# Kernel tuning notes

Hardware: AMD Instinct MI355X
Metric: run time of the kernel (lower is better)

The kernel has to match this reference:

```python
import jax, jax.numpy as jnp
import numpy as np

EPS = 1e-6

def _ln(x, w, b):
    m = x.mean(-1, keepdims=True)
    v = ((x - m) ** 2).mean(-1, keepdims=True)
    return (x - m) / jnp.sqrt(v + EPS) * w + b

def setup_inputs() -> dict:
    key = jax.random.key(0)
    ks = jax.random.split(key, 16)
    N, P, C, M = 8192, 64, 128, 4096
    MW = M * P  # 262144 gathered tokens
    A, BL = 131072, 65536
    x = jax.random.normal(ks[0], (N, P, C), dtype=jnp.float32)
    index_window = jax.random.permutation(ks[1], N)[:M]
    index_partition = jax.random.permutation(ks[2], MW)
    perm2 = jax.random.permutation(ks[3], MW)
    asy_index = perm2[:A]
    blocked_index = perm2[A:A + BL]
    p = lambda k, sh: 0.02 * jax.random.normal(k, sh, dtype=jnp.float32)
    return {
        "x": x,
        "index_window": index_window,
        "index_partition": index_partition,
        "asy_index": asy_index,
        "blocked_index": blocked_index,
        "M": M,
        "B": N,
        "ln1_w": jnp.ones((C,), jnp.float32), "ln1_b": jnp.zeros((C,), jnp.float32),
        "qkv_w": p(ks[4], (C, 3 * C)), "qkv_b": jnp.zeros((3 * C,), jnp.float32),
        "proj_w": p(ks[5], (C, C)), "proj_b": jnp.zeros((C,), jnp.float32),
        "gamma1": jnp.full((C,), 1e-1, jnp.float32),
        "ln2_w": jnp.ones((C,), jnp.float32), "ln2_b": jnp.zeros((C,), jnp.float32),
        "mlp_w1": p(ks[6], (C, 4 * C)), "mlp_b1": jnp.zeros((4 * C,), jnp.float32),
        "mlp_w2": p(ks[7], (4 * C, C)), "mlp_b2": jnp.zeros((C,), jnp.float32),
        "gamma2": jnp.full((C,), 1e-1, jnp.float32),
    }

def reference(x, index_window, index_partition, asy_index, blocked_index, M, B,
              ln1_w, ln1_b, qkv_w, qkv_b, proj_w, proj_b, gamma1,
              ln2_w, ln2_b, mlp_w1, mlp_b1, mlp_w2, mlp_b2, gamma2):
    N, P, C = x.shape
    H, dh = 4, 32
    scale = dh ** -0.5
    MW = index_partition.shape[0]
    x = _ln(x, ln1_w, ln1_b)                      # first_norm over whole input
    X = x                                          # (N, P, C)
    xw = x[index_window].reshape(-1, C)            # gather windows -> (MW, C)
    XX = xw
    xa = _ln(xw[asy_index], ln1_w, ln1_b)          # second norm on asy tokens
    xw = xw.at[asy_index].set(xa)
    shortcut = xa                                  # (A, C)
    xp = xw[index_partition].reshape(M, -1, C)     # (M, P, C) attention groups
    qkv = (xp @ qkv_w + qkv_b).reshape(M, P, H, 3 * dh).transpose(0, 2, 1, 3)
    q, k, v = jnp.split(qkv, 3, axis=3)            # each (M, H, P, dh)
    attn = jnp.einsum('mhqd,mhkd->mhqk', q, k) * scale
    # scatter scores keyed by key-token into flat map, mask blocked keys, gather back
    am = jnp.zeros((MW, P, H), attn.dtype)
    am = am.at[index_partition].set(jnp.transpose(attn, (0, 3, 2, 1)).reshape(MW, P, H))
    am = am.at[blocked_index].set(-10000.0)
    attn = jnp.transpose(am[index_partition].reshape(M, P, P, H), (0, 3, 2, 1))
    attn = jax.nn.softmax(attn, axis=-1)
    o = jnp.einsum('mhqk,mhkd->mhqd', attn, v).transpose(0, 2, 1, 3).reshape(M, P, C)
    o = o @ proj_w + proj_b
    XX = XX.at[index_partition].set(o.reshape(-1, C))
    y = XX[asy_index]
    # sub_layers: [ls1, droppath(id), ln2, mlp, ls2, droppath(id)]
    y = y * gamma1                                 # i=0
    y = shortcut + y                               # i=1 residual
    shortcut = y
    y2 = _ln(y, ln2_w, ln2_b)                      # i=2
    y2 = jax.nn.gelu(y2 @ mlp_w1 + mlp_b1, approximate=False) @ mlp_w2 + mlp_b2  # i=3
    y2 = y2 * gamma2                               # i=4
    y = shortcut + y2                              # i=5 residual
    XX = XX.at[asy_index].set(y)
    XX = XX.at[blocked_index].set(X[index_window].reshape(-1, C)[blocked_index])
    X = X.at[index_window].set(XX.reshape(M, -1, C))
    return X
```

## Files before the change

kernel.cpp:

```cpp
#include <hip/hip_runtime.h>
#include <hip/hip_bf16.h>
#include <math.h>

#define N_   8192
#define P_   64
#define C_   128
#define M_   4096
#define MW_  (M_ * P_)
#define A_   131072
#define BL_  65536
#define NROWS_ (N_ * P_)

typedef __attribute__((ext_vector_type(8))) __bf16 bf16x8;
typedef __attribute__((ext_vector_type(4))) float f32x4;
typedef __attribute__((ext_vector_type(2))) __bf16 bf16x2;

__device__ __forceinline__ float wave_sum(float v) {
#pragma unroll
  for (int o = 32; o > 0; o >>= 1) v += __shfl_xor(v, o, 64);
  return v;
}

__global__ __launch_bounds__(256) void k_set8(unsigned char* p, int n) {
  int i = blockIdx.x * 256 + threadIdx.x;
  if (i < n) p[i] = 0;
}
__global__ __launch_bounds__(256) void k_scatter2(unsigned char* p,
                                                  const int* __restrict__ ia,
                                                  const int* __restrict__ ib) {
  int i = blockIdx.x * 256 + threadIdx.x;
  if (i < A_) p[ia[i]] = 1;
  else {
    int j = i - A_;
    if (j < BL_) p[ib[j]] = 2;
  }
}

__global__ __launch_bounds__(256) void k_prep(const float* __restrict__ qkvw,
                                              const float* __restrict__ projw,
                                              const float* __restrict__ w1,
                                              const float* __restrict__ w2,
                                              __bf16* __restrict__ qkvt,
                                              __bf16* __restrict__ projt,
                                              __bf16* __restrict__ w1t,
                                              __bf16* __restrict__ w2t) {
  int i = blockIdx.x * 256 + threadIdx.x;
  if (i < 384 * 128) {
    int col = i >> 7, row = i & 127;
    qkvt[i] = (__bf16)qkvw[row * 384 + col];
  } else if (i < 384 * 128 + 128 * 128) {
    int j = i - 384 * 128;
    int col = j >> 7, row = j & 127;
    projt[j] = (__bf16)projw[row * 128 + col];
  } else if (i < 384 * 128 + 128 * 128 + 512 * 128) {
    int j = i - 384 * 128 - 128 * 128;
    int col = j >> 7, row = j & 127;
    w1t[j] = (__bf16)w1[row * 512 + col];
  } else {
    int j = i - 384 * 128 - 128 * 128 - 512 * 128;
    int col = j >> 9, row = j & 511;
    w2t[j] = (__bf16)w2[row * 128 + col];
  }
}

__global__ __launch_bounds__(256) void k_ln_all(const float* __restrict__ x,
                                                const float* __restrict__ w,
                                                const float* __restrict__ b,
                                                float* __restrict__ out) {
  int hw = threadIdx.x >> 5, l = threadIdx.x & 31;
  size_t row = (size_t)blockIdx.x * 8 + hw;
  float4 v = ((const float4*)(x + row * 128))[l];
  float s = (v.x + v.y) + (v.z + v.w);
#pragma unroll
  for (int o = 1; o < 32; o <<= 1) s += __shfl_xor(s, o, 64);
  float mean = s * (1.0f / 128.0f);
  float d0 = v.x - mean, d1 = v.y - mean, d2 = v.z - mean, d3 = v.w - mean;
  float q = (d0 * d0 + d1 * d1) + (d2 * d2 + d3 * d3);
#pragma unroll
  for (int o = 1; o < 32; o <<= 1) q += __shfl_xor(q, o, 64);
  float inv = rsqrtf(q * (1.0f / 128.0f) + 1e-6f);
  float4 wv = ((const float4*)w)[l];
  float4 bv = ((const float4*)b)[l];
  float4 o4;
  o4.x = d0 * inv * wv.x + bv.x;
  o4.y = d1 * inv * wv.y + bv.y;
  o4.z = d2 * inv * wv.z + bv.z;
  o4.w = d3 * inv * wv.w + bv.w;
  ((float4*)(out + row * 128))[l] = o4;
}

__global__ __launch_bounds__(512, 6) void k_attn(
    const int* __restrict__ iw,
    const int* __restrict__ ip, const unsigned char* __restrict__ flags,
    const float* __restrict__ ln1w, const float* __restrict__ ln1b,
    const __bf16* __restrict__ qkvt, const float* __restrict__ qkvb,
    const __bf16* __restrict__ projt, const float* __restrict__ projb,
    float* out) {
  __shared__ __align__(16) __bf16 XV[64 * 132];
  __shared__ __align__(16) __bf16 scratch[4 * 4352];
  __shared__ int srow[64];
  __shared__ unsigned char fl[64];

  const int tid = threadIdx.x;
  const int w = tid >> 6, lane = tid & 63;
  const int quad = lane >> 4, cl = lane & 15;
  const int h = w >> 1, mh = w & 1;
  const int m = blockIdx.x;

  if (tid < 64) {
    int s = ip[(m << 6) + tid];
    fl[tid] = flags[s];
    srow[tid] = iw[s >> 6] * 64 + (s & 63);
  }
  __syncthreads();

  __bf16* Xs = XV;
  const float lw0 = ln1w[2 * lane], lw1 = ln1w[2 * lane + 1];
  const float lb0 = ln1b[2 * lane], lb1 = ln1b[2 * lane + 1];

  {
    float2 xv[8];
#pragma unroll
    for (int ii = 0; ii < 8; ++ii) {
      int r = w * 8 + ii;
      xv[ii] = ((const float2*)(out + (size_t)srow[r] * 128))[lane];
    }
#pragma unroll
    for (int ii = 0; ii < 8; ++ii) {
      int r = w * 8 + ii;
      float y0 = xv[ii].x, y1 = xv[ii].y;
      if (fl[r] == 1) {
        float mean = wave_sum(y0 + y1) * (1.0f / 128.0f);
        float d0 = y0 - mean, d1 = y1 - mean;
        float inv = rsqrtf(wave_sum(d0 * d0 + d1 * d1) * (1.0f / 128.0f) + 1e-6f);
        y0 = d0 * inv * lw0 + lb0;
        y1 = d1 * inv * lw1 + lb1;
      }
      bf16x2 p2;
      p2[0] = (__bf16)y0; p2[1] = (__bf16)y1;
      *(bf16x2*)&Xs[r * 132 + 2 * lane] = p2;
    }
  }
  __syncthreads();

  __bf16* wsc = scratch + h * 4352;
  __bf16* Qs  = wsc;
  __bf16* Ks  = wsc + 2176;
  __bf16* Vts = XV + h * 2112;
  __bf16* Ps  = wsc;
  __bf16* Os  = wsc;

  bf16x8 af[2][4];
#pragma unroll
  for (int mtl = 0; mtl < 2; ++mtl)
#pragma unroll
    for (int kt = 0; kt < 4; ++kt)
      af[mtl][kt] = *(const bf16x8*)&Xs[((mh * 2 + mtl) * 16 + cl) * 132 + kt * 32 + quad * 8];
  __syncthreads();

#pragma unroll
  for (int t = 0; t < 3; ++t) {
#pragma unroll
    for (int nt = 0; nt < 2; ++nt) {
      int col = h * 96 + t * 32 + nt * 16 + cl;
      bf16x8 bfr[4];
#pragma unroll
      for (int kt = 0; kt < 4; ++kt)
        bfr[kt] = *(const bf16x8*)&qkvt[(size_t)col * 128 + kt * 32 + quad * 8];
      float bias = qkvb[col];
      __builtin_amdgcn_s_setprio(1);
#pragma unroll
      for (int mtl = 0; mtl < 2; ++mtl) {
        int mt = mh * 2 + mtl;
        f32x4 acc = {bias, bias, bias, bias};
#pragma unroll
        for (int kt = 0; kt < 4; ++kt)
          acc = __builtin_amdgcn_mfma_f32_16x16x32_bf16(af[mtl][kt], bfr[kt], acc, 0, 0, 0);
        if (t == 0) {
#pragma unroll
          for (int r = 0; r < 4; ++r)
            Qs[(mt * 16 + quad * 4 + r) * 34 + nt * 16 + cl] = (__bf16)acc[r];
        } else if (t == 1) {
#pragma unroll
          for (int r = 0; r < 4; ++r)
            Ks[(mt * 16 + quad * 4 + r) * 34 + nt * 16 + cl] = (__bf16)acc[r];
        } else {
#pragma unroll
          for (int r = 0; r < 4; ++r)
            Vts[(nt * 16 + cl) * 66 + mt * 16 + quad * 4 + r] = (__bf16)acc[r];
        }
      }
      __builtin_amdgcn_s_setprio(0);
    }
  }
  __syncthreads();

  f32x4 sc4[2][4];
  {
    bf16x8 bk[4];
#pragma unroll
    for (int nt = 0; nt < 4; ++nt)
      bk[nt] = *(const bf16x8*)&Ks[(nt * 16 + cl) * 34 + quad * 8];
    bf16x8 aq[2];
#pragma unroll
    for (int mtl = 0; mtl < 2; ++mtl)
      aq[mtl] = *(const bf16x8*)&Qs[((mh * 2 + mtl) * 16 + cl) * 34 + quad * 8];
    __builtin_amdgcn_s_setprio(1);
#pragma unroll
    for (int mtl = 0; mtl < 2; ++mtl)
#pragma unroll
      for (int nt = 0; nt < 4; ++nt) {
        f32x4 z = {0.f, 0.f, 0.f, 0.f};
        sc4[mtl][nt] = __builtin_amdgcn_mfma_f32_16x16x32_bf16(aq[mtl], bk[nt], z, 0, 0, 0);
      }
    __builtin_amdgcn_s_setprio(0);
  }
  __syncthreads();

  const float scale = 0.17677669529663687f;
  bool blk[4];
#pragma unroll
  for (int nt = 0; nt < 4; ++nt) blk[nt] = (fl[nt * 16 + cl] == 2);
#pragma unroll
  for (int mtl = 0; mtl < 2; ++mtl)
#pragma unroll
    for (int nt = 0; nt < 4; ++nt)
#pragma unroll
      for (int r = 0; r < 4; ++r) {
        float v = sc4[mtl][nt][r];
        sc4[mtl][nt][r] = blk[nt] ? -10000.0f : v * scale;
      }
#pragma unroll
  for (int mtl = 0; mtl < 2; ++mtl) {
#pragma unroll
    for (int r = 0; r < 4; ++r) {
      float mx = fmaxf(fmaxf(sc4[mtl][0][r], sc4[mtl][1][r]),
                       fmaxf(sc4[mtl][2][r], sc4[mtl][3][r]));
#pragma unroll
      for (int off = 1; off < 16; off <<= 1) mx = fmaxf(mx, __shfl_xor(mx, off, 64));
      float e0 = __expf(sc4[mtl][0][r] - mx);
      float e1 = __expf(sc4[mtl][1][r] - mx);
      float e2 = __expf(sc4[mtl][2][r] - mx);
      float e3 = __expf(sc4[mtl][3][r] - mx);
      float sm = (e0 + e1) + (e2 + e3);
#pragma unroll
      for (int off = 1; off < 16; off <<= 1) sm += __shfl_xor(sm, off, 64);
      float inv = 1.0f / sm;
      int row = (mh * 2 + mtl) * 16 + quad * 4 + r;
      Ps[row * 68 +  0 + cl] = (__bf16)(e0 * inv);
      Ps[row * 68 + 16 + cl] = (__bf16)(e1 * inv);
      Ps[row * 68 + 32 + cl] = (__bf16)(e2 * inv);
      Ps[row * 68 + 48 + cl] = (__bf16)(e3 * inv);
    }
  }

  f32x4 oacc[2][2];
  {
    bf16x8 bv[2][2];
#pragma unroll
    for (int nt = 0; nt < 2; ++nt)
#pragma unroll
      for (int kt = 0; kt < 2; ++kt)
        bv[nt][kt] = *(const bf16x8*)&Vts[(nt * 16 + cl) * 66 + kt * 32 + quad * 8];
    __builtin_amdgcn_s_setprio(1);
#pragma unroll
    for (int mtl = 0; mtl < 2; ++mtl) {
      int mt = mh * 2 + mtl;
      bf16x8 ap0 = *(const bf16x8*)&Ps[(mt * 16 + cl) * 68 + quad * 8];
      bf16x8 ap1 = *(const bf16x8*)&Ps[(mt * 16 + cl) * 68 + 32 + quad * 8];
#pragma unroll
      for (int nt = 0; nt < 2; ++nt) {
        f32x4 z = {0.f, 0.f, 0.f, 0.f};
        z = __builtin_amdgcn_mfma_f32_16x16x32_bf16(ap0, bv[nt][0], z, 0, 0, 0);
        z = __builtin_amdgcn_mfma_f32_16x16x32_bf16(ap1, bv[nt][1], z, 0, 0, 0);
        oacc[mtl][nt] = z;
      }
    }
    __builtin_amdgcn_s_setprio(0);
  }
  __syncthreads();
#pragma unroll
  for (int mtl = 0; mtl < 2; ++mtl)
#pragma unroll
    for (int nt = 0; nt < 2; ++nt)
#pragma unroll
      for (int r = 0; r < 4; ++r)
        Os[((mh * 2 + mtl) * 16 + quad * 4 + r) * 36 + nt * 16 + cl] = (__bf16)oacc[mtl][nt][r];
  __syncthreads();

  {
    const int col = w * 16 + cl;
    bf16x8 bpr[4];
#pragma unroll
    for (int kt = 0; kt < 4; ++kt)
      bpr[kt] = *(const bf16x8*)&projt[(size_t)col * 128 + kt * 32 + quad * 8];
    const float pb = projb[col];
#pragma unroll
    for (int mt = 0; mt < 4; ++mt) {
      f32x4 acc = {pb, pb, pb, pb};
#pragma unroll
      for (int kt = 0; kt < 4; ++kt) {
        const __bf16* op = scratch + kt * 4352;
        bf16x8 a = *(const bf16x8*)&op[(mt * 16 + cl) * 36 + quad * 8];
        acc = __builtin_amdgcn_mfma_f32_16x16x32_bf16(a, bpr[kt], acc, 0, 0, 0);
      }
#pragma unroll
      for (int r = 0; r < 4; ++r) {
        int row = mt * 16 + quad * 4 + r;
        if (fl[row] != 2)
          out[(size_t)srow[row] * 128 + col] = acc[r];
      }
    }
  }
}

__global__ __launch_bounds__(256, 4) void k_mlp(
    const float* __restrict__ x, const int* __restrict__ iw,
    const int* __restrict__ ia,
    const float* __restrict__ ln1w, const float* __restrict__ ln1b,
    const float* __restrict__ g1,
    const float* __restrict__ ln2w, const float* __restrict__ ln2b,
    const __bf16* __restrict__ w1t, const float* __restrict__ b1,
    const __bf16* __restrict__ w2t, const float* __restrict__ b2,
    const float* __restrict__ g2,
    float* out) {
  __shared__ __align__(16) __bf16 y2s[64 * 136];
  __shared__ __align__(16) __bf16 hb[64 * 136];
  __shared__ int wrs[64];

  const int tid = threadIdx.x;
  const int w = tid >> 6, lane = tid & 63;
  const int quad = lane >> 4, cl = lane & 15;

  if (tid < 64) {
    int s = ia[(blockIdx.x << 6) + tid];
    wrs[tid] = iw[s >> 6] * 64 + (s & 63);
  }
  __syncthreads();

  const float lw0 = ln1w[2 * lane], lw1 = ln1w[2 * lane + 1];
  const float lb0 = ln1b[2 * lane], lb1 = ln1b[2 * lane + 1];
  const float g1a = g1[2 * lane], g1b = g1[2 * lane + 1];
  const float l2w0 = ln2w[2 * lane], l2w1 = ln2w[2 * lane + 1];
  const float l2b0 = ln2b[2 * lane], l2b1 = ln2b[2 * lane + 1];

  for (int half = 0; half < 2; ++half) {
    float2 xv[8], ov[8];
#pragma unroll
    for (int ii = 0; ii < 8; ++ii) {
      int r = w + 4 * (half * 8 + ii);
      size_t wr = (size_t)wrs[r];
      xv[ii] = ((const float2*)(x + wr * 128))[lane];
      ov[ii] = ((const float2*)(out + wr * 128))[lane];
    }
#pragma unroll
    for (int ii = 0; ii < 8; ++ii) {
      int r = w + 4 * (half * 8 + ii);
      float mean = wave_sum(xv[ii].x + xv[ii].y) * (1.0f / 128.0f);
      float d0 = xv[ii].x - mean, d1 = xv[ii].y - mean;
      float inv = rsqrtf(wave_sum(d0 * d0 + d1 * d1) * (1.0f / 128.0f) + 1e-6f);
      float y0 = d0 * inv * lw0 + lb0, y1 = d1 * inv * lw1 + lb1;
      mean = wave_sum(y0 + y1) * (1.0f / 128.0f);
      d0 = y0 - mean; d1 = y1 - mean;
      inv = rsqrtf(wave_sum(d0 * d0 + d1 * d1) * (1.0f / 128.0f) + 1e-6f);
      float xa0 = d0 * inv * lw0 + lb0, xa1 = d1 * inv * lw1 + lb1;
      float yv0 = xa0 + g1a * ov[ii].x;
      float yv1 = xa1 + g1b * ov[ii].y;
      ((float2*)(out + (size_t)wrs[r] * 128))[lane] = make_float2(yv0, yv1);
      mean = wave_sum(yv0 + yv1) * (1.0f / 128.0f);
      d0 = yv0 - mean; d1 = yv1 - mean;
      inv = rsqrtf(wave_sum(d0 * d0 + d1 * d1) * (1.0f / 128.0f) + 1e-6f);
      bf16x2 p2;
      p2[0] = (__bf16)(d0 * inv * l2w0 + l2b0);
      p2[1] = (__bf16)(d1 * inv * l2w1 + l2b1);
      *(bf16x2*)&y2s[r * 136 + 2 * lane] = p2;
    }
  }
  __threadfence_block();
  __syncthreads();

  f32x4 zacc[4][2];
#pragma unroll
  for (int nt = 0; nt < 2; ++nt) {
    float bb = b2[w * 32 + nt * 16 + cl];
#pragma unroll
    for (int mt = 0; mt < 4; ++mt) zacc[mt][nt] = (f32x4){bb, bb, bb, bb};
  }

  for (int ch = 0; ch < 4; ++ch) {
#pragma unroll
    for (int nt = 0; nt < 2; ++nt) {
      int col = ch * 128 + w * 32 + nt * 16 + cl;
      bf16x8 bfr[4];
#pragma unroll
      for (int kt = 0; kt < 4; ++kt)
        bfr[kt] = *(const bf16x8*)&w1t[(size_t)col * 128 + kt * 32 + quad * 8];
      float bias = b1[col];
      __builtin_amdgcn_s_setprio(1);
#pragma unroll
      for (int mt = 0; mt < 4; ++mt) {
        f32x4 acc = {bias, bias, bias, bias};
#pragma unroll
        for (int kt = 0; kt < 4; ++kt) {
          bf16x8 a = *(const bf16x8*)&y2s[(mt * 16 + cl) * 136 + kt * 32 + quad * 8];
          acc = __builtin_amdgcn_mfma_f32_16x16x32_bf16(a, bfr[kt], acc, 0, 0, 0);
        }
#pragma unroll
        for (int r = 0; r < 4; ++r) {
          float a = acc[r];
          float g = a * 0.5f * (1.0f + erff(a * 0.70710678118654752f));
          hb[(mt * 16 + quad * 4 + r) * 136 + w * 32 + nt * 16 + cl] = (__bf16)g;
        }
      }
      __builtin_amdgcn_s_setprio(0);
    }
    __syncthreads();
#pragma unroll
    for (int nt = 0; nt < 2; ++nt) {
      int col = w * 32 + nt * 16 + cl;
      bf16x8 bfr[4];
#pragma unroll
      for (int kk = 0; kk < 4; ++kk)
        bfr[kk] = *(const bf16x8*)&w2t[(size_t)col * 512 + ch * 128 + kk * 32 + quad * 8];
      __builtin_amdgcn_s_setprio(1);
#pragma unroll
      for (int mt = 0; mt < 4; ++mt)
#pragma unroll
        for (int kk = 0; kk < 4; ++kk) {
          bf16x8 a = *(const bf16x8*)&hb[(mt * 16 + cl) * 136 + kk * 32 + quad * 8];
          zacc[mt][nt] = __builtin_amdgcn_mfma_f32_16x16x32_bf16(a, bfr[kk],
                                                                zacc[mt][nt], 0, 0, 0);
        }
      __builtin_amdgcn_s_setprio(0);
    }
    __syncthreads();
  }

#pragma unroll
  for (int mt = 0; mt < 4; ++mt)
#pragma unroll
    for (int nt = 0; nt < 2; ++nt) {
      int col = w * 32 + nt * 16 + cl;
      float gg = g2[col];
#pragma unroll
      for (int r = 0; r < 4; ++r) {
        int row = mt * 16 + quad * 4 + r;
        size_t a = (size_t)wrs[row] * 128 + col;
        out[a] = out[a] + gg * zacc[mt][nt][r];
      }
    }
}

extern "C" void kernel_launch(void* const* d_in, const int* in_sizes, int n_in,
                              void* d_out, int out_size, void* d_ws, size_t ws_size,
                              hipStream_t stream) {
  const float* x = (const float*)d_in[0];
  const int* iw = (const int*)d_in[1];
  const int* ip = (const int*)d_in[2];
  const int* ia = (const int*)d_in[3];
  const int* ib = (const int*)d_in[4];
  const float* ln1w = (const float*)d_in[7];
  const float* ln1b = (const float*)d_in[8];
  const float* qkvw = (const float*)d_in[9];
  const float* qkvb = (const float*)d_in[10];
  const float* projw = (const float*)d_in[11];
  const float* projb = (const float*)d_in[12];
  const float* g1 = (const float*)d_in[13];
  const float* ln2w = (const float*)d_in[14];
  const float* ln2b = (const float*)d_in[15];
  const float* w1 = (const float*)d_in[16];
  const float* b1 = (const float*)d_in[17];
  const float* w2 = (const float*)d_in[18];
  const float* b2 = (const float*)d_in[19];
  const float* g2 = (const float*)d_in[20];
  float* out = (float*)d_out;

  unsigned char* flags = (unsigned char*)d_ws;
  __bf16* qkvt = (__bf16*)((char*)d_ws + MW_);
  __bf16* projt = (__bf16*)((char*)d_ws + MW_ + 384 * 128 * 2);
  __bf16* w1t = (__bf16*)((char*)d_ws + MW_ + 384 * 128 * 2 + 128 * 128 * 2);
  __bf16* w2t = (__bf16*)((char*)d_ws + MW_ + 384 * 128 * 2 + 128 * 128 * 2 + 512 * 128 * 2);

  k_set8<<<MW_ / 256, 256, 0, stream>>>(flags, MW_);
  k_scatter2<<<(A_ + BL_) / 256, 256, 0, stream>>>(flags, ia, ib);
  k_prep<<<(384 * 128 + 128 * 128 + 512 * 128 + 128 * 512) / 256, 256, 0, stream>>>(
      qkvw, projw, w1, w2, qkvt, projt, w1t, w2t);
  k_ln_all<<<NROWS_ / 8, 256, 0, stream>>>(x, ln1w, ln1b, out);
  k_attn<<<M_, 512, 0, stream>>>(iw, ip, flags, ln1w, ln1b, qkvt, qkvb,
                                 projt, projb, out);
  k_mlp<<<A_ / 64, 256, 0, stream>>>(x, iw, ia, ln1w, ln1b, g1, ln2w, ln2b,
                                     w1t, b1, w2t, b2, g2, out);
}
```

Baseline: 838.8 us.

## Fuse first residual into attention epilogue and shrink MLP hidden chunk buffer

The attention kernel now saves the second-LayerNorm statistics for asy rows and applies the gamma1-scaled residual directly in its projection epilogue. This lets the MLP kernel skip re-reading x and recomputing two LayerNorms. The MLP hidden buffer is halved by processing eight 64-wide chunks instead of four 128-wide ones, aimed at raising occupancy, at the cost of more barriers. Launch bounds also change: attention goes from 6 to 4 and MLP from 4 to 5, and the extra epilogue read-modify-write may add register pressure in the attention kernel.

```diff
diff --git a/kernel.cpp b/kernel.cpp
--- a/kernel.cpp
+++ b/kernel.cpp
@@ -89,17 +89,20 @@
   ((float4*)(out + row * 128))[l] = o4;
 }
 
-__global__ __launch_bounds__(512, 6) void k_attn(
+__global__ __launch_bounds__(512, 4) void k_attn(
     const int* __restrict__ iw,
     const int* __restrict__ ip, const unsigned char* __restrict__ flags,
     const float* __restrict__ ln1w, const float* __restrict__ ln1b,
     const __bf16* __restrict__ qkvt, const float* __restrict__ qkvb,
     const __bf16* __restrict__ projt, const float* __restrict__ projb,
+    const float* __restrict__ g1,
     float* out) {
   __shared__ __align__(16) __bf16 XV[64 * 132];
   __shared__ __align__(16) __bf16 scratch[4 * 4352];
   __shared__ int srow[64];
   __shared__ unsigned char fl[64];
+  __shared__ float sm2[64];
+  __shared__ float si2[64];
 
   const int tid = threadIdx.x;
   const int w = tid >> 6, lane = tid & 63;
@@ -133,6 +136,7 @@
         float mean = wave_sum(y0 + y1) * (1.0f / 128.0f);
         float d0 = y0 - mean, d1 = y1 - mean;
         float inv = rsqrtf(wave_sum(d0 * d0 + d1 * d1) * (1.0f / 128.0f) + 1e-6f);
+        if (lane == 0) { sm2[r] = mean; si2[r] = inv; }
         y0 = d0 * inv * lw0 + lb0;
         y1 = d1 * inv * lw1 + lb1;
       }
@@ -290,6 +294,7 @@
 
   {
     const int col = w * 16 + cl;
+    const float lwc = ln1w[col], lbc = ln1b[col], g1c = g1[col];
     bf16x8 bpr[4];
 #pragma unroll
     for (int kt = 0; kt < 4; ++kt)
@@ -307,25 +312,29 @@
 #pragma unroll
       for (int r = 0; r < 4; ++r) {
         int row = mt * 16 + quad * 4 + r;
-        if (fl[row] != 2)
+        unsigned char f = fl[row];
+        if (f == 0) {
           out[(size_t)srow[row] * 128 + col] = acc[r];
-      }
-    }
-  }
-}
-
-__global__ __launch_bounds__(256, 4) void k_mlp(
-    const float* __restrict__ x, const int* __restrict__ iw,
-    const int* __restrict__ ia,
-    const float* __restrict__ ln1w, const float* __restrict__ ln1b,
-    const float* __restrict__ g1,
+        } else if (f == 1) {
+          size_t a = (size_t)srow[row] * 128 + col;
+          float lnv = out[a];
+          float xa = (lnv - sm2[row]) * si2[row] * lwc + lbc;
+          out[a] = xa + g1c * acc[r];
+        }
+      }
+    }
+  }
+}
+
+__global__ __launch_bounds__(256, 5) void k_mlp(
+    const int* __restrict__ iw, const int* __restrict__ ia,
     const float* __restrict__ ln2w, const float* __restrict__ ln2b,
     const __bf16* __restrict__ w1t, const float* __restrict__ b1,
     const __bf16* __restrict__ w2t, const float* __restrict__ b2,
     const float* __restrict__ g2,
     float* out) {
   __shared__ __align__(16) __bf16 y2s[64 * 136];
-  __shared__ __align__(16) __bf16 hb[64 * 136];
+  __shared__ __align__(16) __bf16 hb[64 * 68];
   __shared__ int wrs[64];
 
   const int tid = threadIdx.x;
@@ -338,45 +347,28 @@
   }
   __syncthreads();
 
-  const float lw0 = ln1w[2 * lane], lw1 = ln1w[2 * lane + 1];
-  const float lb0 = ln1b[2 * lane], lb1 = ln1b[2 * lane + 1];
-  const float g1a = g1[2 * lane], g1b = g1[2 * lane + 1];
   const float l2w0 = ln2w[2 * lane], l2w1 = ln2w[2 * lane + 1];
   const float l2b0 = ln2b[2 * lane], l2b1 = ln2b[2 * lane + 1];
 
   for (int half = 0; half < 2; ++half) {
-    float2 xv[8], ov[8];
+    float2 yv[8];
 #pragma unroll
     for (int ii = 0; ii < 8; ++ii) {
       int r = w + 4 * (half * 8 + ii);
-      size_t wr = (size_t)wrs[r];
-      xv[ii] = ((const float2*)(x + wr * 128))[lane];
-      ov[ii] = ((const float2*)(out + wr * 128))[lane];
+      yv[ii] = ((const float2*)(out + (size_t)wrs[r] * 128))[lane];
     }
 #pragma unroll
     for (int ii = 0; ii < 8; ++ii) {
       int r = w + 4 * (half * 8 + ii);
-      float mean = wave_sum(xv[ii].x + xv[ii].y) * (1.0f / 128.0f);
-      float d0 = xv[ii].x - mean, d1 = xv[ii].y - mean;
+      float mean = wave_sum(yv[ii].x + yv[ii].y) * (1.0f / 128.0f);
+      float d0 = yv[ii].x - mean, d1 = yv[ii].y - mean;
       float inv = rsqrtf(wave_sum(d0 * d0 + d1 * d1) * (1.0f / 128.0f) + 1e-6f);
-      float y0 = d0 * inv * lw0 + lb0, y1 = d1 * inv * lw1 + lb1;
-      mean = wave_sum(y0 + y1) * (1.0f / 128.0f);
-      d0 = y0 - mean; d1 = y1 - mean;
-      inv = rsqrtf(wave_sum(d0 * d0 + d1 * d1) * (1.0f / 128.0f) + 1e-6f);
-      float xa0 = d0 * inv * lw0 + lb0, xa1 = d1 * inv * lw1 + lb1;
-      float yv0 = xa0 + g1a * ov[ii].x;
-      float yv1 = xa1 + g1b * ov[ii].y;
-      ((float2*)(out + (size_t)wrs[r] * 128))[lane] = make_float2(yv0, yv1);
-      mean = wave_sum(yv0 + yv1) * (1.0f / 128.0f);
-      d0 = yv0 - mean; d1 = yv1 - mean;
-      inv = rsqrtf(wave_sum(d0 * d0 + d1 * d1) * (1.0f / 128.0f) + 1e-6f);
       bf16x2 p2;
       p2[0] = (__bf16)(d0 * inv * l2w0 + l2b0);
       p2[1] = (__bf16)(d1 * inv * l2w1 + l2b1);
       *(bf16x2*)&y2s[r * 136 + 2 * lane] = p2;
     }
   }
-  __threadfence_block();
   __syncthreads();
 
   f32x4 zacc[4][2];
@@ -387,10 +379,9 @@
     for (int mt = 0; mt < 4; ++mt) zacc[mt][nt] = (f32x4){bb, bb, bb, bb};
   }
 
-  for (int ch = 0; ch < 4; ++ch) {
-#pragma unroll
-    for (int nt = 0; nt < 2; ++nt) {
-      int col = ch * 128 + w * 32 + nt * 16 + cl;
+  for (int ch = 0; ch < 8; ++ch) {
+    {
+      int col = ch * 64 + w * 16 + cl;
       bf16x8 bfr[4];
 #pragma unroll
       for (int kt = 0; kt < 4; ++kt)
@@ -409,7 +400,7 @@
         for (int r = 0; r < 4; ++r) {
           float a = acc[r];
           float g = a * 0.5f * (1.0f + erff(a * 0.70710678118654752f));
-          hb[(mt * 16 + quad * 4 + r) * 136 + w * 32 + nt * 16 + cl] = (__bf16)g;
+          hb[(mt * 16 + quad * 4 + r) * 68 + w * 16 + cl] = (__bf16)g;
         }
       }
       __builtin_amdgcn_s_setprio(0);
@@ -418,16 +409,16 @@
 #pragma unroll
     for (int nt = 0; nt < 2; ++nt) {
       int col = w * 32 + nt * 16 + cl;
-      bf16x8 bfr[4];
-#pragma unroll
-      for (int kk = 0; kk < 4; ++kk)
-        bfr[kk] = *(const bf16x8*)&w2t[(size_t)col * 512 + ch * 128 + kk * 32 + quad * 8];
+      bf16x8 bfr[2];
+#pragma unroll
+      for (int kk = 0; kk < 2; ++kk)
+        bfr[kk] = *(const bf16x8*)&w2t[(size_t)col * 512 + ch * 64 + kk * 32 + quad * 8];
       __builtin_amdgcn_s_setprio(1);
 #pragma unroll
       for (int mt = 0; mt < 4; ++mt)
 #pragma unroll
-        for (int kk = 0; kk < 4; ++kk) {
-          bf16x8 a = *(const bf16x8*)&hb[(mt * 16 + cl) * 136 + kk * 32 + quad * 8];
+        for (int kk = 0; kk < 2; ++kk) {
+          bf16x8 a = *(const bf16x8*)&hb[(mt * 16 + cl) * 68 + kk * 32 + quad * 8];
           zacc[mt][nt] = __builtin_amdgcn_mfma_f32_16x16x32_bf16(a, bfr[kk],
                                                                 zacc[mt][nt], 0, 0, 0);
         }
@@ -487,7 +478,7 @@
       qkvw, projw, w1, w2, qkvt, projt, w1t, w2t);
   k_ln_all<<<NROWS_ / 8, 256, 0, stream>>>(x, ln1w, ln1b, out);
   k_attn<<<M_, 512, 0, stream>>>(iw, ip, flags, ln1w, ln1b, qkvt, qkvb,
-                                 projt, projb, out);
-  k_mlp<<<A_ / 64, 256, 0, stream>>>(x, iw, ia, ln1w, ln1b, g1, ln2w, ln2b,
+                                 projt, projb, g1, out);
+  k_mlp<<<A_ / 64, 256, 0, stream>>>(iw, ia, ln2w, ln2b,
                                      w1t, b1, w2t, b2, g2, out);
 }
```

After: 858.1 us. +2.3%, slower.
